# Kernel optimization log

Hardware: AMD Instinct MI355X
Metric: run time of the kernel (lower is better)

Reference implementation:

```python
import jax, jax.numpy as jnp
import numpy as np

N, E, CIN, H, OUT, L, G = 100000, 1600000, 64, 128, 16, 3, 64

def setup_inputs() -> dict:
    key = jax.random.key(0)
    ks = jax.random.split(key, 20)
    def xav(k, shape):
        fan_in, fan_out = shape[-2], shape[-1]
        lim = float(np.sqrt(6.0 / (fan_in + fan_out)))
        return jax.random.uniform(k, shape, jnp.float32, -lim, lim)
    inp = {
        "x": jax.random.normal(ks[0], (N, CIN), jnp.float32),
        "pos": jax.random.normal(ks[1], (N, 3), jnp.float32),
        "edge_index": jax.random.randint(ks[2], (2, E), 0, N, jnp.int64),
        "batch": jnp.sort(jax.random.randint(ks[3], (N,), 0, G, jnp.int64)),
        # node_lin: Linear(CIN+3, H) -> ReLU -> Linear(H, H)
        "node_w1": xav(ks[4], (CIN + 3, H)), "node_b1": jnp.zeros((H,), jnp.float32),
        "node_w2": xav(ks[5], (H, H)), "node_b2": jnp.zeros((H,), jnp.float32),
        # L convs, each with [L, H, H] propagation weights and a GRUCell
        "conv_w": xav(ks[6], (L, L, H, H)),
        "gru_wih": xav(ks[7], (L, 3 * H, H)), "gru_whh": xav(ks[8], (L, 3 * H, H)),
        "gru_bih": jnp.zeros((L, 3 * H), jnp.float32), "gru_bhh": jnp.zeros((L, 3 * H), jnp.float32),
        "lin1_w": xav(ks[9], (H, H // 2)), "lin1_b": jnp.zeros((H // 2,), jnp.float32),
        "lin2_w": xav(ks[10], (H // 2, OUT)), "lin2_b": jnp.zeros((OUT,), jnp.float32),
    }
    return inp

def _gru_cell(m, h, wih, whh, bih, bhh):
    # torch.nn.GRUCell semantics: gates = [r, z, n]
    gi = m @ wih.T + bih  # [N, 3H]
    gh = h @ whh.T + bhh
    ir, iz, inn = jnp.split(gi, 3, axis=1)
    hr, hz, hn = jnp.split(gh, 3, axis=1)
    r = jax.nn.sigmoid(ir + hr)
    z = jax.nn.sigmoid(iz + hz)
    n = jnp.tanh(inn + r * hn)
    return (1.0 - z) * n + z * h

def reference(x, pos, edge_index, batch, node_w1, node_b1, node_w2, node_b2,
              conv_w, gru_wih, gru_whh, gru_bih, gru_bhh,
              lin1_w, lin1_b, lin2_w, lin2_b):
    src, dst = edge_index[0], edge_index[1]  # message flows src -> dst
    h = jnp.concatenate([x, pos], axis=1)
    h = jax.nn.relu(h @ node_w1 + node_b1) @ node_w2 + node_b2
    for l in range(L):  # GatedNet outer convs
        for i in range(L):  # GatedGraphConv inner iterations
            m = h @ conv_w[l, i]                                  # [N, H]
            agg = jax.ops.segment_sum(m[src], dst, num_segments=N)  # gather + scatter-add
            h = _gru_cell(agg, h, gru_wih[l], gru_whh[l], gru_bih[l], gru_bhh[l])
        h = jax.nn.relu(h)
    h = jax.nn.relu(h @ lin1_w + lin1_b)
    h = h @ lin2_w + lin2_b                                        # [N, OUT]
    return jax.ops.segment_sum(h, batch, num_segments=G)           # graph readout 'add'
```

## Files before the change

kernel.cpp:

```cpp
#include <hip/hip_runtime.h>

#define NN 100000
#define NE 1600000
#define NG 64
#define MAXDEG 64

typedef long long i64;
typedef unsigned short u16;
typedef unsigned int u32;
typedef __attribute__((ext_vector_type(8))) _Float16 f16x8;
typedef __attribute__((ext_vector_type(4))) _Float16 half4;
typedef __attribute__((ext_vector_type(4))) float f32x4;

__device__ __forceinline__ float sigm(float x){ return 1.f/(1.f+__expf(-x)); }
__device__ __forceinline__ float tanh_(float x){ return 2.f/(1.f+__expf(-2.f*x)) - 1.f; }
__device__ __forceinline__ f32x4 mfma16h(f16x8 a, f16x8 b, f32x4 c){
  return __builtin_amdgcn_mfma_f32_16x16x32_f16(a,b,c,0,0,0);
}
__device__ __forceinline__ u16 h2u(_Float16 h){ return *(const u16*)&h; }

__global__ __launch_bounds__(512) void k_detect(const int* __restrict__ ei,
    const int* __restrict__ batch, int* __restrict__ flags){
  int t = threadIdx.x;
  __shared__ int nz_e, nz_b;
  if (t == 0){ nz_e = 0; nz_b = 0; }
  __syncthreads();
  if (ei[2*t + 1] != 0) nz_e = 1;
  int k = NN/2 - 512 + t;
  if (batch[2*k + 1] != 0) nz_b = 1;
  __syncthreads();
  if (t == 0){ flags[0] = nz_e ? 0 : 1; flags[1] = nz_b ? 0 : 1; }
}

__global__ __launch_bounds__(256) void k_prep_wT(const float* __restrict__ wih,
    const float* __restrict__ whh, float* __restrict__ wihT, float* __restrict__ whhT){
  int idx = blockIdx.x*256 + threadIdx.x;
  if (idx >= 3*49152) return;
  int l = idx/49152, r = idx - l*49152, k = r/384, jc = r - k*384;
  wihT[idx] = wih[((size_t)l*384 + jc)*128 + k];
  whhT[idx] = whh[((size_t)l*384 + jc)*128 + k];
}

__global__ __launch_bounds__(384) void k_weff(const float* __restrict__ convw,
    const float* __restrict__ wihT, float* __restrict__ WeffT){
  int bid = blockIdx.x;
  int li = bid >> 7, k = bid & 127;
  int l = li / 3;
  int j = threadIdx.x;
  __shared__ float cwrow[128];
  if (j < 128) cwrow[j] = convw[((size_t)li*128 + k)*128 + j];
  __syncthreads();
  const float* wT = wihT + (size_t)l*49152;
  float acc = 0.f;
#pragma unroll 8
  for (int m = 0; m < 128; ++m)
    acc = fmaf(cwrow[m], wT[(size_t)m*384 + j], acc);
  WeffT[(size_t)li*49152 + (size_t)k*384 + j] = acc;
}

__global__ __launch_bounds__(256) void k_bsplit(const float* __restrict__ WeffT,
    const float* __restrict__ whhT, u16* __restrict__ Bhi, u16* __restrict__ Blo){
  int idx = blockIdx.x*256 + threadIdx.x;
  int li = idx >> 17;
  int r = idx & 131071;
  int col = r >> 8, k = r & 255;
  int l = li / 3;
  float v = 0.f;
  if (k < 128){
    if (col < 384) v = WeffT[(size_t)li*49152 + (size_t)k*384 + col];
  } else {
    int k2 = k - 128;
    if (col < 256)       v = whhT[(size_t)l*49152 + (size_t)k2*384 + col];
    else if (col >= 384) v = whhT[(size_t)l*49152 + (size_t)k2*384 + (col-128)];
  }
  _Float16 hi = (_Float16)v;
  _Float16 lo = (_Float16)(v - (float)hi);
  size_t widx = (size_t)li*131072 + ((((size_t)(k>>5))*512 + col)*4 + ((k>>3)&3))*8 + (k&7);
  Bhi[widx] = h2u(hi);
  Blo[widx] = h2u(lo);
}

__global__ __launch_bounds__(256) void k_fill_edges(const int* __restrict__ ei,
    const int* __restrict__ flags, int* __restrict__ deg, int* __restrict__ col){
  int e = blockIdx.x*256 + threadIdx.x;
  if (e >= NE) return;
  int s, d;
  if (flags[0]){
    const i64* e64 = (const i64*)ei;
    s = (int)e64[e]; d = (int)e64[NE + e];
  } else {
    s = ei[e]; d = ei[NE + e];
  }
  int slot = atomicAdd(&deg[d], 1);
  if (slot < MAXDEG) col[(size_t)d*MAXDEG + slot] = s;
}

__global__ __launch_bounds__(128) void k_enc_n(const float* __restrict__ x,
    const float* __restrict__ pos, const float* __restrict__ w1, const float* __restrict__ b1,
    const float* __restrict__ w2, const float* __restrict__ b2, float* __restrict__ h){
  int n0 = blockIdx.x * 8, j = threadIdx.x;
  __shared__ float xr[8][68];
  __shared__ float t1[8][128];
  for (int q = j; q < 8*67; q += 128){
    int p = q/67, kk = q - p*67;
    xr[p][kk] = (kk < 64) ? x[(size_t)(n0+p)*64 + kk] : pos[(size_t)(n0+p)*3 + (kk-64)];
  }
  __syncthreads();
  float s[8];
#pragma unroll
  for (int p=0;p<8;++p) s[p] = b1[j];
  for (int k=0;k<67;++k){
    float w = w1[k*128 + j];
#pragma unroll
    for (int p=0;p<8;++p) s[p] = fmaf(xr[p][k], w, s[p]);
  }
#pragma unroll
  for (int p=0;p<8;++p) t1[p][j] = fmaxf(s[p], 0.f);
  __syncthreads();
#pragma unroll
  for (int p=0;p<8;++p) s[p] = b2[j];
  for (int k=0;k<128;++k){
    float w = w2[k*128 + j];
#pragma unroll
    for (int p=0;p<8;++p) s[p] = fmaf(t1[p][k], w, s[p]);
  }
#pragma unroll
  for (int p=0;p<8;++p) h[(size_t)(n0+p)*128 + j] = s[p];
}

__global__ __launch_bounds__(512, 8) void k_fused(const int* __restrict__ deg,
    const int* __restrict__ col, const float* __restrict__ hin, float* __restrict__ hout,
    const u16* __restrict__ Bhi, const u16* __restrict__ Blo,
    const float* __restrict__ bih, const float* __restrict__ bhh, int apply_relu){
  __shared__ u16 Ahi[32*256];
  __shared__ u16 Alo[32*256];
  const int tid = threadIdx.x, lane = tid & 63, w = tid >> 6;
  const int tile = blockIdx.x * 32;

#pragma unroll
  for (int i = 0; i < 2; ++i){
    int f = i*512 + tid;
    int row = f >> 5, colq = f & 31;
    float4 v = *(const float4*)(hin + (size_t)(tile+row)*128 + colq*4);
    int colu = 128 + colq*4;
    int cs = (colu >> 3) ^ (row & 7);
    int idx = row*256 + cs*8 + (colu & 7);
    _Float16 h0=(_Float16)v.x, h1=(_Float16)v.y, h2=(_Float16)v.z, h3=(_Float16)v.w;
    _Float16 l0=(_Float16)(v.x-(float)h0), l1=(_Float16)(v.y-(float)h1),
             l2=(_Float16)(v.z-(float)h2), l3=(_Float16)(v.w-(float)h3);
    half4 hv = {h0,h1,h2,h3};
    half4 lv = {l0,l1,l2,l3};
    *(half4*)(Ahi + idx) = hv;
    *(half4*)(Alo + idx) = lv;
  }

  const int half = lane >> 5, ln32 = lane & 31;
#pragma unroll
  for (int rr = 0; rr < 2; ++rr){
    int row = rr*16 + w*2 + half;
    int node = tile + row;
    int d = deg[node]; d = min(d, MAXDEG);
    int src1 = col[(size_t)node*MAXDEG + ln32];
    int src2 = col[(size_t)node*MAXDEG + 32 + ln32];
    float ax=0.f, ay=0.f, az=0.f, aw=0.f;
    int d1 = min(d, 32);
    int s = 0;
    for (; s + 3 < d1; s += 4){
      int a0 = __shfl(src1, half*32 + s, 64);
      int a1 = __shfl(src1, half*32 + s + 1, 64);
      int a2 = __shfl(src1, half*32 + s + 2, 64);
      int a3 = __shfl(src1, half*32 + s + 3, 64);
      float4 v0 = *(const float4*)(hin + (size_t)a0*128 + (ln32<<2));
      float4 v1 = *(const float4*)(hin + (size_t)a1*128 + (ln32<<2));
      float4 v2 = *(const float4*)(hin + (size_t)a2*128 + (ln32<<2));
      float4 v3 = *(const float4*)(hin + (size_t)a3*128 + (ln32<<2));
      ax += v0.x + v1.x + v2.x + v3.x;
      ay += v0.y + v1.y + v2.y + v3.y;
      az += v0.z + v1.z + v2.z + v3.z;
      aw += v0.w + v1.w + v2.w + v3.w;
    }
    for (; s < d1; ++s){
      int a0 = __shfl(src1, half*32 + s, 64);
      float4 v0 = *(const float4*)(hin + (size_t)a0*128 + (ln32<<2));
      ax += v0.x; ay += v0.y; az += v0.z; aw += v0.w;
    }
    int d2 = d - d1;
    s = 0;
    for (; s + 3 < d2; s += 4){
      int a0 = __shfl(src2, half*32 + s, 64);
      int a1 = __shfl(src2, half*32 + s + 1, 64);
      int a2 = __shfl(src2, half*32 + s + 2, 64);
      int a3 = __shfl(src2, half*32 + s + 3, 64);
      float4 v0 = *(const float4*)(hin + (size_t)a0*128 + (ln32<<2));
      float4 v1 = *(const float4*)(hin + (size_t)a1*128 + (ln32<<2));
      float4 v2 = *(const float4*)(hin + (size_t)a2*128 + (ln32<<2));
      float4 v3 = *(const float4*)(hin + (size_t)a3*128 + (ln32<<2));
      ax += v0.x + v1.x + v2.x + v3.x;
      ay += v0.y + v1.y + v2.y + v3.y;
      az += v0.z + v1.z + v2.z + v3.z;
      aw += v0.w + v1.w + v2.w + v3.w;
    }
    for (; s < d2; ++s){
      int a0 = __shfl(src2, half*32 + s, 64);
      float4 v0 = *(const float4*)(hin + (size_t)a0*128 + (ln32<<2));
      ax += v0.x; ay += v0.y; az += v0.z; aw += v0.w;
    }
    int colu = ln32 << 2;
    int cs = (colu >> 3) ^ (row & 7);
    int idx = row*256 + cs*8 + (colu & 7);
    _Float16 hx=(_Float16)ax, hy=(_Float16)ay, hz=(_Float16)az, hw=(_Float16)aw;
    _Float16 lx=(_Float16)(ax-(float)hx), ly=(_Float16)(ay-(float)hy),
             lz=(_Float16)(az-(float)hz), lw=(_Float16)(aw-(float)hw);
    half4 hv = {hx,hy,hz,hw};
    half4 lv = {lx,ly,lz,lw};
    *(half4*)(Ahi + idx) = hv;
    *(half4*)(Alo + idx) = lv;
  }
  __syncthreads();

  const f32x4 fz = {0.f,0.f,0.f,0.f};
  f32x4 acc[4][2];
#pragma unroll
  for (int g=0;g<4;++g)
#pragma unroll
    for (int R=0;R<2;++R) acc[g][R] = fz;

#pragma unroll
  for (int kk = 0; kk < 8; ++kk){
    f16x8 a_hi[2], a_lo[2];
#pragma unroll
    for (int R=0;R<2;++R){
      int arow = R*16 + (lane&15);
      int cs = (kk*4 + (lane>>4)) ^ (arow & 7);
      a_hi[R] = *(const f16x8*)(Ahi + arow*256 + cs*8);
      a_lo[R] = *(const f16x8*)(Alo + arow*256 + cs*8);
    }
#pragma unroll
    for (int g=0; g<4; ++g){
      if (g==2 && kk>=4) continue;
      if (g==3 && kk<4) continue;
      int colg = g*128 + w*16 + (lane&15);
      size_t boff = (((size_t)kk*512 + colg)*4 + (lane>>4))*8;
      f16x8 bh = *(const f16x8*)(Bhi + boff);
      f16x8 bl = *(const f16x8*)(Blo + boff);
#pragma unroll
      for (int R=0;R<2;++R){
        acc[g][R] = mfma16h(a_hi[R], bh, acc[g][R]);
        acc[g][R] = mfma16h(a_hi[R], bl, acc[g][R]);
        acc[g][R] = mfma16h(a_lo[R], bh, acc[g][R]);
      }
    }
  }

  float hn_reg[2][4];
  {
    int jj = w*16 + (lane&15);
    float br  = bih[jj]     + bhh[jj];
    float bz  = bih[128+jj] + bhh[128+jj];
    float bin = bih[256+jj];
    float bhn = bhh[256+jj];
#pragma unroll
    for (int R=0;R<2;++R)
#pragma unroll
      for (int v=0;v<4;++v){
        int r_ = R*16 + ((lane>>4)<<2) + v;
        float rg = sigm(acc[0][R][v] + br);
        float zg = sigm(acc[1][R][v] + bz);
        float hnv = acc[3][R][v] + bhn;
        float ng = tanh_(acc[2][R][v] + bin + rg*hnv);
        int colu = 128 + jj;
        int cs = (colu >> 3) ^ (r_ & 7);
        int lidx = r_*256 + cs*8 + (colu & 7);
        float hold = (float)(*(const _Float16*)(Ahi + lidx))
                   + (float)(*(const _Float16*)(Alo + lidx));
        float hnew = (1.f - zg)*ng + zg*hold;
        if (apply_relu) hnew = fmaxf(hnew, 0.f);
        hn_reg[R][v] = hnew;
      }
  }
  __syncthreads();
  float* fout = (float*)Ahi;
  {
    int jj = w*16 + (lane&15);
#pragma unroll
    for (int R=0;R<2;++R)
#pragma unroll
      for (int v=0;v<4;++v){
        int r_ = R*16 + ((lane>>4)<<2) + v;
        fout[r_*128 + jj] = hn_reg[R][v];
      }
  }
  __syncthreads();
#pragma unroll
  for (int i = 0; i < 2; ++i){
    int f = i*512 + tid;
    int row = f >> 5, colq = f & 31;
    float4 vv = *(const float4*)(fout + row*128 + colq*4);
    *(float4*)(hout + (size_t)(tile+row)*128 + colq*4) = vv;
  }
}

__global__ __launch_bounds__(64) void k_head_n(const float* __restrict__ h,
    const float* __restrict__ l1, const float* __restrict__ b1,
    const float* __restrict__ l2, const float* __restrict__ b2, float* __restrict__ nodeout){
  int n0 = blockIdx.x * 8, j = threadIdx.x;
  __shared__ float hrow[8][128], t[8][64];
  for (int q = j; q < 1024; q += 64){
    int p = q >> 7, k = q & 127;
    hrow[p][k] = h[(size_t)(n0+p)*128 + k];
  }
  __syncthreads();
  float s[8];
#pragma unroll
  for (int p=0;p<8;++p) s[p] = b1[j];
  for (int k=0;k<128;++k){
    float w = l1[k*64 + j];
#pragma unroll
    for (int p=0;p<8;++p) s[p] = fmaf(hrow[p][k], w, s[p]);
  }
#pragma unroll
  for (int p=0;p<8;++p) t[p][j] = fmaxf(s[p], 0.f);
  __syncthreads();
  int c = j & 15;
#pragma unroll
  for (int pp=0;pp<2;++pp){
    int p = (j >> 4) + pp*4;
    float o = b2[c];
    for (int k=0;k<64;++k) o = fmaf(t[p][k], l2[k*16 + c], o);
    nodeout[(size_t)(n0+p)*16 + c] = o;
  }
}

__device__ __forceinline__ int lbound32(const int* __restrict__ a, int n, int v){
  int lo = 0, hi = n;
  while (lo < hi){ int mid = (lo+hi)>>1; if (a[mid] < v) lo = mid+1; else hi = mid; }
  return lo;
}
__device__ __forceinline__ int lbound64(const i64* __restrict__ a, int n, i64 v){
  int lo = 0, hi = n;
  while (lo < hi){ int mid = (lo+hi)>>1; if (a[mid] < v) lo = mid+1; else hi = mid; }
  return lo;
}
__global__ __launch_bounds__(256) void k_reduce(const float* __restrict__ nodeout,
    const int* __restrict__ batch, const int* __restrict__ flags, float* __restrict__ out){
  int g = blockIdx.x;
  int lo, hi;
  if (flags[1]){
    const i64* b64 = (const i64*)batch;
    lo = lbound64(b64, NN, (i64)g); hi = lbound64(b64, NN, (i64)g+1);
  } else {
    lo = lbound32(batch, NN, g); hi = lbound32(batch, NN, g+1);
  }
  int tid = threadIdx.x;
  int c = tid & 15, rr = tid >> 4;
  float s = 0.f;
  for (int r = lo + rr; r < hi; r += 16) s += nodeout[(size_t)r*16 + c];
  __shared__ float red[256];
  red[tid] = s; __syncthreads();
  for (int step = 128; step >= 16; step >>= 1){
    if (tid < step) red[tid] += red[tid + step];
    __syncthreads();
  }
  if (tid < 16) out[g*16 + tid] = red[tid];
}

extern "C" void kernel_launch(void* const* d_in, const int* in_sizes, int n_in,
                              void* d_out, int out_size, void* d_ws, size_t ws_size,
                              hipStream_t stream){
  const float* x        = (const float*)d_in[0];
  const float* pos      = (const float*)d_in[1];
  const int*   edge     = (const int*)d_in[2];
  const int*   batch    = (const int*)d_in[3];
  const float* node_w1  = (const float*)d_in[4];
  const float* node_b1  = (const float*)d_in[5];
  const float* node_w2  = (const float*)d_in[6];
  const float* node_b2  = (const float*)d_in[7];
  const float* conv_w   = (const float*)d_in[8];
  const float* gru_wih  = (const float*)d_in[9];
  const float* gru_whh  = (const float*)d_in[10];
  const float* gru_bih  = (const float*)d_in[11];
  const float* gru_bhh  = (const float*)d_in[12];
  const float* lin1_w   = (const float*)d_in[13];
  const float* lin1_b   = (const float*)d_in[14];
  const float* lin2_w   = (const float*)d_in[15];
  const float* lin2_b   = (const float*)d_in[16];
  float* out = (float*)d_out;

  char* p = (char*)d_ws;
  int*   flags = (int*)p;   p += 256;
  float* h0    = (float*)p; p += (size_t)NN*128*4;
  float* h1    = (float*)p; p += (size_t)NN*128*4;
  float* nodeout = (float*)p; p += (size_t)NN*16*4;
  int*   deg   = (int*)p;   p += (size_t)NN*4;
  int*   col   = (int*)p;   p += (size_t)NN*MAXDEG*4;
  float* wihT  = (float*)p; p += (size_t)3*49152*4;
  float* whhT  = (float*)p; p += (size_t)3*49152*4;
  float* WeffT = (float*)p; p += (size_t)9*49152*4;
  u16*   Bhi   = (u16*)p;   p += (size_t)9*512*256*2;
  u16*   Blo   = (u16*)p;   p += (size_t)9*512*256*2;

  k_detect<<<1, 512, 0, stream>>>(edge, batch, flags);
  hipMemsetAsync(deg, 0, (size_t)NN*4, stream);
  k_prep_wT<<<(147456 + 255)/256, 256, 0, stream>>>(gru_wih, gru_whh, wihT, whhT);
  k_weff<<<9*128, 384, 0, stream>>>(conv_w, wihT, WeffT);
  k_bsplit<<<9*512*256/256, 256, 0, stream>>>(WeffT, whhT, Bhi, Blo);
  k_fill_edges<<<NE/256, 256, 0, stream>>>(edge, flags, deg, col);
  k_enc_n<<<NN/8, 128, 0, stream>>>(x, pos, node_w1, node_b1, node_w2, node_b2, h0);

  float* hbuf[2] = { h0, h1 };
  for (int l = 0; l < 3; ++l){
    for (int i = 0; i < 3; ++i){
      int li = l*3 + i;
      k_fused<<<NN/32, 512, 0, stream>>>(deg, col, hbuf[li & 1], hbuf[(li + 1) & 1],
          Bhi + (size_t)li*131072, Blo + (size_t)li*131072,
          gru_bih + l*384, gru_bhh + l*384, (i==2) ? 1 : 0);
    }
  }
  k_head_n<<<NN/8, 64, 0, stream>>>(hbuf[1], lin1_w, lin1_b, lin2_w, lin2_b, nodeout);
  k_reduce<<<NG, 256, 0, stream>>>(nodeout, batch, flags, out);
}
```

Before: 1.902 ms.

## Move node encoder MLP to split-fp16 MFMA and deepen gather unroll

Replaces the scalar-FMA node encoder kernel with an MFMA version. It splits the inputs and weights into fp16 hi/lo pairs and uses three MFMAs per product to keep near-fp32 accuracy, with weights pre-packed by a new prep kernel. It also widens the first neighbour-gather loop in the fused conv kernel from 4 to 8 loads in flight to raise memory-level parallelism. The encoder runs once and is small next to the nine fused conv launches, so the main gain depends on the gather unroll, which costs extra registers.

```diff
diff --git a/kernel.cpp b/kernel.cpp
--- a/kernel.cpp
+++ b/kernel.cpp
@@ -80,6 +80,30 @@
   Blo[widx] = h2u(lo);
 }
 
+__global__ __launch_bounds__(256) void k_bsplit_enc(const float* __restrict__ w1,
+    const float* __restrict__ w2, u16* __restrict__ B1hi, u16* __restrict__ B1lo,
+    u16* __restrict__ B2hi, u16* __restrict__ B2lo){
+  int idx = blockIdx.x*256 + threadIdx.x;
+  if (idx < 12288){
+    int j = idx / 96, k = idx - j*96;
+    float v = (k < 67) ? w1[k*128 + j] : 0.f;
+    _Float16 hi = (_Float16)v;
+    _Float16 lo = (_Float16)(v - (float)hi);
+    size_t widx = ((((size_t)(k>>5))*128 + j)*4 + ((k>>3)&3))*8 + (k&7);
+    B1hi[widx] = h2u(hi);
+    B1lo[widx] = h2u(lo);
+  } else {
+    int r = idx - 12288;
+    int j = r >> 7, k = r & 127;
+    float v = w2[k*128 + j];
+    _Float16 hi = (_Float16)v;
+    _Float16 lo = (_Float16)(v - (float)hi);
+    size_t widx = ((((size_t)(k>>5))*128 + j)*4 + ((k>>3)&3))*8 + (k&7);
+    B2hi[widx] = h2u(hi);
+    B2lo[widx] = h2u(lo);
+  }
+}
+
 __global__ __launch_bounds__(256) void k_fill_edges(const int* __restrict__ ei,
     const int* __restrict__ flags, int* __restrict__ deg, int* __restrict__ col){
   int e = blockIdx.x*256 + threadIdx.x;
@@ -95,37 +119,138 @@
   if (slot < MAXDEG) col[(size_t)d*MAXDEG + slot] = s;
 }
 
-__global__ __launch_bounds__(128) void k_enc_n(const float* __restrict__ x,
-    const float* __restrict__ pos, const float* __restrict__ w1, const float* __restrict__ b1,
-    const float* __restrict__ w2, const float* __restrict__ b2, float* __restrict__ h){
-  int n0 = blockIdx.x * 8, j = threadIdx.x;
-  __shared__ float xr[8][68];
-  __shared__ float t1[8][128];
-  for (int q = j; q < 8*67; q += 128){
-    int p = q/67, kk = q - p*67;
-    xr[p][kk] = (kk < 64) ? x[(size_t)(n0+p)*64 + kk] : pos[(size_t)(n0+p)*3 + (kk-64)];
-  }
-  __syncthreads();
-  float s[8];
-#pragma unroll
-  for (int p=0;p<8;++p) s[p] = b1[j];
-  for (int k=0;k<67;++k){
-    float w = w1[k*128 + j];
-#pragma unroll
-    for (int p=0;p<8;++p) s[p] = fmaf(xr[p][k], w, s[p]);
-  }
-#pragma unroll
-  for (int p=0;p<8;++p) t1[p][j] = fmaxf(s[p], 0.f);
-  __syncthreads();
-#pragma unroll
-  for (int p=0;p<8;++p) s[p] = b2[j];
-  for (int k=0;k<128;++k){
-    float w = w2[k*128 + j];
-#pragma unroll
-    for (int p=0;p<8;++p) s[p] = fmaf(t1[p][k], w, s[p]);
-  }
-#pragma unroll
-  for (int p=0;p<8;++p) h[(size_t)(n0+p)*128 + j] = s[p];
+__global__ __launch_bounds__(512, 8) void k_enc_mfma(const float* __restrict__ x,
+    const float* __restrict__ pos,
+    const u16* __restrict__ B1hi, const u16* __restrict__ B1lo,
+    const u16* __restrict__ B2hi, const u16* __restrict__ B2lo,
+    const float* __restrict__ b1, const float* __restrict__ b2, float* __restrict__ h){
+  __shared__ u16 lds[4*32*128];
+  u16* Ahi = lds;            u16* Alo = lds + 4096;
+  u16* Thi = lds + 8192;     u16* Tlo = lds + 12288;
+  const int tid = threadIdx.x, lane = tid & 63, w = tid >> 6;
+  const int tile = blockIdx.x * 32;
+
+  {
+    int o = tid * 8;
+    half4 z = {0,0,0,0};
+    *(half4*)(Ahi + o) = z;  *(half4*)(Ahi + o + 4) = z;
+    *(half4*)(Alo + o) = z;  *(half4*)(Alo + o + 4) = z;
+  }
+  __syncthreads();
+
+  {
+    int row = tid >> 4, colq = tid & 15;
+    float4 v = *(const float4*)(x + (size_t)(tile+row)*64 + colq*4);
+    int colu = colq*4;
+    int cs = (colu >> 3) ^ (row & 7);
+    int idx = row*128 + cs*8 + (colu & 7);
+    _Float16 h0=(_Float16)v.x, h1=(_Float16)v.y, h2=(_Float16)v.z, h3=(_Float16)v.w;
+    _Float16 l0=(_Float16)(v.x-(float)h0), l1=(_Float16)(v.y-(float)h1),
+             l2=(_Float16)(v.z-(float)h2), l3=(_Float16)(v.w-(float)h3);
+    half4 hv = {h0,h1,h2,h3};
+    half4 lv = {l0,l1,l2,l3};
+    *(half4*)(Ahi + idx) = hv;
+    *(half4*)(Alo + idx) = lv;
+  }
+  if (tid < 32){
+    int row = tid;
+    int n = tile + row;
+    float p0 = pos[(size_t)n*3], p1 = pos[(size_t)n*3+1], p2 = pos[(size_t)n*3+2];
+    _Float16 h0=(_Float16)p0, h1=(_Float16)p1, h2=(_Float16)p2;
+    _Float16 l0=(_Float16)(p0-(float)h0), l1=(_Float16)(p1-(float)h1), l2=(_Float16)(p2-(float)h2);
+    int cs = 8 ^ (row & 7);
+    int idx = row*128 + cs*8;
+    half4 hv = {h0,h1,h2,(_Float16)0.f};
+    half4 lv = {l0,l1,l2,(_Float16)0.f};
+    *(half4*)(Ahi + idx) = hv;
+    *(half4*)(Alo + idx) = lv;
+  }
+  __syncthreads();
+
+  const f32x4 fz = {0.f,0.f,0.f,0.f};
+  f32x4 acc1[2] = {fz, fz};
+#pragma unroll
+  for (int kk = 0; kk < 3; ++kk){
+    f16x8 a_hi[2], a_lo[2];
+#pragma unroll
+    for (int R=0;R<2;++R){
+      int arow = R*16 + (lane&15);
+      int cs = (kk*4 + (lane>>4)) ^ (arow & 7);
+      a_hi[R] = *(const f16x8*)(Ahi + arow*128 + cs*8);
+      a_lo[R] = *(const f16x8*)(Alo + arow*128 + cs*8);
+    }
+    int colg = w*16 + (lane&15);
+    size_t boff = (((size_t)kk*128 + colg)*4 + (lane>>4))*8;
+    f16x8 bh = *(const f16x8*)(B1hi + boff);
+    f16x8 bl = *(const f16x8*)(B1lo + boff);
+#pragma unroll
+    for (int R=0;R<2;++R){
+      acc1[R] = mfma16h(a_hi[R], bh, acc1[R]);
+      acc1[R] = mfma16h(a_hi[R], bl, acc1[R]);
+      acc1[R] = mfma16h(a_lo[R], bh, acc1[R]);
+    }
+  }
+  {
+    int jj = w*16 + (lane&15);
+    float bias1 = b1[jj];
+#pragma unroll
+    for (int R=0;R<2;++R)
+#pragma unroll
+      for (int v=0;v<4;++v){
+        int r_ = R*16 + ((lane>>4)<<2) + v;
+        float t = fmaxf(acc1[R][v] + bias1, 0.f);
+        _Float16 hi = (_Float16)t;
+        _Float16 lo = (_Float16)(t - (float)hi);
+        int cs = (jj >> 3) ^ (r_ & 7);
+        int idx = r_*128 + cs*8 + (jj & 7);
+        Thi[idx] = h2u(hi);
+        Tlo[idx] = h2u(lo);
+      }
+  }
+  __syncthreads();
+
+  f32x4 acc2[2] = {fz, fz};
+#pragma unroll
+  for (int kk = 0; kk < 4; ++kk){
+    f16x8 a_hi[2], a_lo[2];
+#pragma unroll
+    for (int R=0;R<2;++R){
+      int arow = R*16 + (lane&15);
+      int cs = (kk*4 + (lane>>4)) ^ (arow & 7);
+      a_hi[R] = *(const f16x8*)(Thi + arow*128 + cs*8);
+      a_lo[R] = *(const f16x8*)(Tlo + arow*128 + cs*8);
+    }
+    int colg = w*16 + (lane&15);
+    size_t boff = (((size_t)kk*128 + colg)*4 + (lane>>4))*8;
+    f16x8 bh = *(const f16x8*)(B2hi + boff);
+    f16x8 bl = *(const f16x8*)(B2lo + boff);
+#pragma unroll
+    for (int R=0;R<2;++R){
+      acc2[R] = mfma16h(a_hi[R], bh, acc2[R]);
+      acc2[R] = mfma16h(a_hi[R], bl, acc2[R]);
+      acc2[R] = mfma16h(a_lo[R], bh, acc2[R]);
+    }
+  }
+  float* fout = (float*)lds;
+  {
+    int jj = w*16 + (lane&15);
+    float bias2 = b2[jj];
+#pragma unroll
+    for (int R=0;R<2;++R)
+#pragma unroll
+      for (int v=0;v<4;++v){
+        int r_ = R*16 + ((lane>>4)<<2) + v;
+        fout[r_*128 + jj] = acc2[R][v] + bias2;
+      }
+  }
+  __syncthreads();
+#pragma unroll
+  for (int i = 0; i < 2; ++i){
+    int f = i*512 + tid;
+    int row = f >> 5, colq = f & 31;
+    float4 vv = *(const float4*)(fout + row*128 + colq*4);
+    *(float4*)(h + (size_t)(tile+row)*128 + colq*4) = vv;
+  }
 }
 
 __global__ __launch_bounds__(512, 8) void k_fused(const int* __restrict__ deg,
@@ -165,19 +290,27 @@
     float ax=0.f, ay=0.f, az=0.f, aw=0.f;
     int d1 = min(d, 32);
     int s = 0;
-    for (; s + 3 < d1; s += 4){
-      int a0 = __shfl(src1, half*32 + s, 64);
+    for (; s + 7 < d1; s += 8){
+      int a0 = __shfl(src1, half*32 + s,     64);
       int a1 = __shfl(src1, half*32 + s + 1, 64);
       int a2 = __shfl(src1, half*32 + s + 2, 64);
       int a3 = __shfl(src1, half*32 + s + 3, 64);
+      int a4 = __shfl(src1, half*32 + s + 4, 64);
+      int a5 = __shfl(src1, half*32 + s + 5, 64);
+      int a6 = __shfl(src1, half*32 + s + 6, 64);
+      int a7 = __shfl(src1, half*32 + s + 7, 64);
       float4 v0 = *(const float4*)(hin + (size_t)a0*128 + (ln32<<2));
       float4 v1 = *(const float4*)(hin + (size_t)a1*128 + (ln32<<2));
       float4 v2 = *(const float4*)(hin + (size_t)a2*128 + (ln32<<2));
       float4 v3 = *(const float4*)(hin + (size_t)a3*128 + (ln32<<2));
-      ax += v0.x + v1.x + v2.x + v3.x;
-      ay += v0.y + v1.y + v2.y + v3.y;
-      az += v0.z + v1.z + v2.z + v3.z;
-      aw += v0.w + v1.w + v2.w + v3.w;
+      float4 v4 = *(const float4*)(hin + (size_t)a4*128 + (ln32<<2));
+      float4 v5 = *(const float4*)(hin + (size_t)a5*128 + (ln32<<2));
+      float4 v6 = *(const float4*)(hin + (size_t)a6*128 + (ln32<<2));
+      float4 v7 = *(const float4*)(hin + (size_t)a7*128 + (ln32<<2));
+      ax += v0.x + v1.x + v2.x + v3.x + v4.x + v5.x + v6.x + v7.x;
+      ay += v0.y + v1.y + v2.y + v3.y + v4.y + v5.y + v6.y + v7.y;
+      az += v0.z + v1.z + v2.z + v3.z + v4.z + v5.z + v6.z + v7.z;
+      aw += v0.w + v1.w + v2.w + v3.w + v4.w + v5.w + v6.w + v7.w;
     }
     for (; s < d1; ++s){
       int a0 = __shfl(src1, half*32 + s, 64);
@@ -187,7 +320,7 @@
     int d2 = d - d1;
     s = 0;
     for (; s + 3 < d2; s += 4){
-      int a0 = __shfl(src2, half*32 + s, 64);
+      int a0 = __shfl(src2, half*32 + s,     64);
       int a1 = __shfl(src2, half*32 + s + 1, 64);
       int a2 = __shfl(src2, half*32 + s + 2, 64);
       int a3 = __shfl(src2, half*32 + s + 3, 64);
@@ -398,14 +531,20 @@
   float* WeffT = (float*)p; p += (size_t)9*49152*4;
   u16*   Bhi   = (u16*)p;   p += (size_t)9*512*256*2;
   u16*   Blo   = (u16*)p;   p += (size_t)9*512*256*2;
+  u16*   B1hi  = (u16*)p;   p += 12288*2;
+  u16*   B1lo  = (u16*)p;   p += 12288*2;
+  u16*   B2hi  = (u16*)p;   p += 16384*2;
+  u16*   B2lo  = (u16*)p;   p += 16384*2;
 
   k_detect<<<1, 512, 0, stream>>>(edge, batch, flags);
   hipMemsetAsync(deg, 0, (size_t)NN*4, stream);
   k_prep_wT<<<(147456 + 255)/256, 256, 0, stream>>>(gru_wih, gru_whh, wihT, whhT);
   k_weff<<<9*128, 384, 0, stream>>>(conv_w, wihT, WeffT);
   k_bsplit<<<9*512*256/256, 256, 0, stream>>>(WeffT, whhT, Bhi, Blo);
+  k_bsplit_enc<<<(12288+16384)/256, 256, 0, stream>>>(node_w1, node_w2, B1hi, B1lo, B2hi, B2lo);
   k_fill_edges<<<NE/256, 256, 0, stream>>>(edge, flags, deg, col);
-  k_enc_n<<<NN/8, 128, 0, stream>>>(x, pos, node_w1, node_b1, node_w2, node_b2, h0);
+  k_enc_mfma<<<NN/32, 512, 0, stream>>>(x, pos, B1hi, B1lo, B2hi, B2lo,
+      node_b1, node_b2, h0);
 
   float* hbuf[2] = { h0, h1 };
   for (int l = 0; l < 3; ++l){
```

Measured after the change: 1.883 ms. No clear change (-1.0%).
